# Kernel tuning notes

Measured on AMD Instinct MI355X. Metric: run time of the kernel, lower is better.

## Reference

```python
import jax, jax.numpy as jnp
import numpy as np

N, M = 20000, 5000
D_IN, D_OUT = 256, 512
EPS = 1e-5


def setup_inputs() -> dict:
    key = jax.random.key(0)
    k1, k2, k3, k4 = jax.random.split(key, 4)
    x = jax.random.normal(k1, (N, D_IN), dtype=jnp.float32)
    H = (jax.random.uniform(k2, (N, M)) < 0.05).astype(jnp.float32)
    W_node = jax.random.normal(k3, (D_IN, D_OUT), dtype=jnp.float32) / np.sqrt(D_IN)
    W_res = jax.random.normal(k4, (D_IN, D_OUT), dtype=jnp.float32) / np.sqrt(D_IN)
    gamma = jnp.ones((D_OUT,), dtype=jnp.float32)
    beta = jnp.zeros((D_OUT,), dtype=jnp.float32)
    return {"x": x, "H": H, "W_node": W_node, "W_res": W_res, "gamma": gamma, "beta": beta}


def reference(x, H, W_node, W_res, gamma, beta):
    # degrees, clamped to >= 1
    d_v = jnp.clip(jnp.sum(H, axis=1), 1.0)   # [N] node degree
    d_e = jnp.clip(jnp.sum(H, axis=0), 1.0)   # [M] hyperedge degree
    x_proj = x @ W_node                       # [N, d_out]
    edge_feat = (H.T @ x_proj) / d_e[:, None] # [M, d_out] node -> edge aggregation
    node_update = (H @ edge_feat) / d_v[:, None]  # [N, d_out] edge -> node
    h = node_update + x @ W_res               # residual (d_in != d_out -> linear)
    # LayerNorm over last dim
    mu = jnp.mean(h, axis=-1, keepdims=True)
    var = jnp.mean(jnp.square(h - mu), axis=-1, keepdims=True)
    out = (h - mu) * jax.lax.rsqrt(var + EPS) * gamma + beta
    return out  # dropout is identity at inference
```

## Files before the change

### kernel.cpp

```cpp
#include <hip/hip_runtime.h>


#define N_NODES 20000
#define M_EDGES 5000
#define MPAD    5120
#define NPAD    20480
#define NW      320
#define MW      80
#define DIN     256
#define DOUT    512
#define SPLITS  16
#define SPLITSB 4

typedef short bf16x8 __attribute__((ext_vector_type(8)));
typedef float f32x4 __attribute__((ext_vector_type(4)));
typedef unsigned long long u64;

#define MFMA16(A, B, C) __builtin_amdgcn_mfma_f32_16x16x32_bf16((A), (B), (C), 0, 0, 0)

__device__ __forceinline__ unsigned short f2b(float f) {
  unsigned u = __builtin_bit_cast(unsigned, f);
  return (unsigned short)((u + 0x7FFFu + ((u >> 16) & 1u)) >> 16);
}

__device__ __forceinline__ float b2f(unsigned short b) {
  return __builtin_bit_cast(float, ((unsigned)b) << 16);
}

__device__ __forceinline__ void stage16(const void* g, void* l) {
  __builtin_amdgcn_global_load_lds(
      (const __attribute__((address_space(1))) unsigned int*)g,
      (__attribute__((address_space(3))) unsigned int*)l, 16, 0, 0);
}

__device__ __forceinline__ bf16x8 expand8(unsigned b) {
  union { unsigned u[4]; bf16x8 v; } r;
  const unsigned t = b | (b << 15);
  r.u[0] = (t & 0x00010001u) * 0x3F80u;
  r.u[1] = ((t >> 2) & 0x00010001u) * 0x3F80u;
  r.u[2] = ((t >> 4) & 0x00010001u) * 0x3F80u;
  r.u[3] = ((t >> 6) & 0x00010001u) * 0x3F80u;
  return r.v;
}

__global__ __launch_bounds__(256) void prep_kernel(const float* __restrict__ Wn,
                                                   const float* __restrict__ Wr,
                                                   unsigned short* __restrict__ wtpb) {
  const int q = blockIdx.x * 256 + threadIdx.x;
  const int j = q >> 9, k = q & 511;
  const float v = (k < 256) ? Wn[(size_t)k * 512 + j] : Wr[(size_t)(k - 256) * 512 + j];
  wtpb[(((size_t)(k >> 3) * 512 + j) << 3) + (k & 7)] = f2b(v);
}

__global__ __launch_bounds__(256) void xt_kernel(const float* __restrict__ x,
                                                 unsigned short* __restrict__ xpb) {
  const int j = threadIdx.x;
  const int n8 = blockIdx.x;
  union { unsigned u[4]; bf16x8 v; } o;
#pragma unroll
  for (int p = 0; p < 4; ++p) {
    const int n = n8 * 8 + 2 * p;
    const float v0 = (n < N_NODES) ? x[(size_t)n * DIN + j] : 0.f;
    const float v1 = (n + 1 < N_NODES) ? x[(size_t)(n + 1) * DIN + j] : 0.f;
    o.u[p] = (unsigned)f2b(v0) | ((unsigned)f2b(v1) << 16);
  }
  *(bf16x8*)(xpb + ((size_t)n8 * 256 + j) * 8) = o.v;
}

__global__ __launch_bounds__(256) void pack_kernel(const float* __restrict__ H,
                                                   u64* __restrict__ HTb) {
  const int t = threadIdx.x;
  const int g = blockIdx.x;
  const int h = blockIdx.y;
  const int n0 = g * 64;
  const int mc = h * 1024 + 4 * t;
  u64 h0 = 0, h1 = 0, h2 = 0, h3 = 0;
  if (mc + 3 < M_EDGES) {
    const float* col = H + mc;
#pragma unroll 4
    for (int r = 0; r < 64; ++r) {
      const int n = n0 + r;
      if (n < N_NODES) {
        const float4 v = *(const float4*)(col + (size_t)n * M_EDGES);
        h0 |= (u64)(v.x != 0.f) << r;
        h1 |= (u64)(v.y != 0.f) << r;
        h2 |= (u64)(v.z != 0.f) << r;
        h3 |= (u64)(v.w != 0.f) << r;
      }
    }
  } else if (mc < M_EDGES) {
    for (int r = 0; r < 64; ++r) {
      const int n = n0 + r;
      if (n < N_NODES) {
        const float* row = H + (size_t)n * M_EDGES;
        if (mc + 0 < M_EDGES) h0 |= (u64)(row[mc + 0] != 0.f) << r;
        if (mc + 1 < M_EDGES) h1 |= (u64)(row[mc + 1] != 0.f) << r;
        if (mc + 2 < M_EDGES) h2 |= (u64)(row[mc + 2] != 0.f) << r;
        if (mc + 3 < M_EDGES) h3 |= (u64)(row[mc + 3] != 0.f) << r;
      }
    }
  }
  u64* hp = HTb + (size_t)g * MPAD + mc;
  hp[0] = h0; hp[1] = h1; hp[2] = h2; hp[3] = h3;
}

__global__ __launch_bounds__(256) void bt_kernel(const u64* __restrict__ HTb,
                                                 u64* __restrict__ Hb) {
  const int t = threadIdx.x;
  const int w = t >> 6, l = t & 63;
  const int id = blockIdx.x * 4 + w;
  const int nw = id % NW;
  const int mw = id / NW;
  const u64 word = HTb[(size_t)nw * MPAD + mw * 64 + l];
  u64 out = 0;
  for (int r = 0; r < 64; ++r) {
    const u64 mask = __ballot(((word >> r) & 1ull) != 0);
    if (l == r) out = mask;
  }
  Hb[(size_t)mw * NPAD + nw * 64 + l] = out;
}

__global__ __launch_bounds__(256) void deg_kernel(const u64* __restrict__ Hb,
                                                  const u64* __restrict__ HTb,
                                                  float* __restrict__ inv_de,
                                                  float* __restrict__ inv_dv) {
  const int g = blockIdx.x * 256 + threadIdx.x;
  if (g < MPAD) {
    int c = 0;
    for (int nw = 0; nw < NW; ++nw) c += __popcll(HTb[(size_t)nw * MPAD + g]);
    inv_de[g] = 1.f / fmaxf((float)c, 1.f);
  } else if (g < MPAD + NPAD) {
    const int n = g - MPAD;
    int c = 0;
#pragma unroll
    for (int mw = 0; mw < MW; ++mw) c += __popcll(Hb[(size_t)mw * NPAD + n]);
    inv_dv[n] = 1.f / fmaxf((float)c, 1.f);
  }
}

__global__ __launch_bounds__(256) void gemmA_kernel(const unsigned short* __restrict__ xpb,
                                                    const u64* __restrict__ HTb,
                                                    unsigned short* __restrict__ partial) {
  __shared__ char lds[2][16384];
  const int t = threadIdx.x;
  const int w = t >> 6, l = t & 63;
  const int lr = l & 15, lg = l >> 4;
  const int shl8 = lg * 8;
  const int wgid = blockIdx.x;
  const int mchunk = wgid >> 6;
  const int sj = wgid & 63;
  const int s = sj >> 2, jb = sj & 3;
  const int m0 = mchunk * 256 + w * 64;
  const int j0 = jb * 64;

  f32x4 acc[4][4] = {};
  const u64* bbase = HTb + (size_t)(s * 20) * MPAD + m0 + lr;
  const char* xb = (const char*)xpb;
  const int n8b = s * 160;
  const int sj0 = j0 + w * 16 + lr;

  u64 b00, b01, b02, b03, b04, b05, b06, b07;
  u64 b10, b11, b12, b13, b14, b15, b16, b17;

#define GA_LOADB(S, st_) do {                                                  \
    const u64* bp_ = bbase + (size_t)(st_) * 2 * MPAD;                         \
    b##S##0 = bp_[0]; b##S##1 = bp_[16]; b##S##2 = bp_[32]; b##S##3 = bp_[48]; \
    const u64* bq_ = bp_ + MPAD;                                               \
    b##S##4 = bq_[0]; b##S##5 = bq_[16]; b##S##6 = bq_[32]; b##S##7 = bq_[48]; \
  } while (0)

#define GA_STAGE(buf, st_) do {                                                \
    const size_t r0_ = (size_t)(n8b + (st_) * 16 + lg) * 256 + sj0;            \
    stage16(xb + (r0_) * 16,              &lds[buf][(w) * 1024 + l * 16]);     \
    stage16(xb + (r0_ + 4 * 256) * 16,    &lds[buf][(4 + w) * 1024 + l * 16]); \
    stage16(xb + (r0_ + 8 * 256) * 16,    &lds[buf][(8 + w) * 1024 + l * 16]); \
    stage16(xb + (r0_ + 12 * 256) * 16,   &lds[buf][(12 + w) * 1024 + l * 16]);\
  } while (0)

#define GA_JG(jg, BW) do {                                                     \
    const unsigned wlo_ = (unsigned)(BW), whi_ = (unsigned)((BW) >> 32);       \
    const bf16x8 e0_ = expand8((wlo_ >> shl8) & 255u);                         \
    const bf16x8 e1_ = expand8((whi_ >> shl8) & 255u);                         \
    acc[0][jg] = MFMA16(A00_, e0_, acc[0][jg]);                                \
    acc[1][jg] = MFMA16(A10_, e0_, acc[1][jg]);                                \
    acc[2][jg] = MFMA16(A20_, e0_, acc[2][jg]);                                \
    acc[3][jg] = MFMA16(A30_, e0_, acc[3][jg]);                                \
    acc[0][jg] = MFMA16(A01_, e1_, acc[0][jg]);                                \
    acc[1][jg] = MFMA16(A11_, e1_, acc[1][jg]);                                \
    acc[2][jg] = MFMA16(A21_, e1_, acc[2][jg]);                                \
    acc[3][jg] = MFMA16(A31_, e1_, acc[3][jg]);                                \
  } while (0)

#define GA_COMP(buf, h, W0, W1, W2, W3) do {                                   \
    const char* L_ = &lds[buf][(h) * 8192];                                    \
    const bf16x8 A00_ = *(const bf16x8*)(L_ + l * 16 + 0);                     \
    const bf16x8 A10_ = *(const bf16x8*)(L_ + l * 16 + 1024);                  \
    const bf16x8 A20_ = *(const bf16x8*)(L_ + l * 16 + 2048);                  \
    const bf16x8 A30_ = *(const bf16x8*)(L_ + l * 16 + 3072);                  \
    const bf16x8 A01_ = *(const bf16x8*)(L_ + l * 16 + 4096);                  \
    const bf16x8 A11_ = *(const bf16x8*)(L_ + l * 16 + 5120);                  \
    const bf16x8 A21_ = *(const bf16x8*)(L_ + l * 16 + 6144);                  \
    const bf16x8 A31_ = *(const bf16x8*)(L_ + l * 16 + 7168);                  \
    GA_JG(0, W0); GA_JG(1, W1); GA_JG(2, W2); GA_JG(3, W3);                    \
  } while (0)

  GA_LOADB(0, 0);
  GA_STAGE(0, 0);
  for (int st = 0; st < 10; st += 2) {
    const int n1 = (st + 1 < 10) ? st + 1 : 9;
    GA_LOADB(1, n1); GA_STAGE(1, n1);
    asm volatile("s_waitcnt vmcnt(12)" ::: "memory");
    __builtin_amdgcn_s_barrier();
    GA_COMP(0, 0, b00, b01, b02, b03);
    GA_COMP(0, 1, b04, b05, b06, b07);
    __builtin_amdgcn_s_barrier();
    const int n2 = (st + 2 < 10) ? st + 2 : 9;
    GA_LOADB(0, n2); GA_STAGE(0, n2);
    asm volatile("s_waitcnt vmcnt(12)" ::: "memory");
    __builtin_amdgcn_s_barrier();
    GA_COMP(1, 0, b10, b11, b12, b13);
    GA_COMP(1, 1, b14, b15, b16, b17);
    __builtin_amdgcn_s_barrier();
  }
#undef GA_LOADB
#undef GA_STAGE
#undef GA_JG
#undef GA_COMP

  unsigned short* pp = partial + (size_t)s * (DIN * MPAD);
#pragma unroll
  for (int fr = 0; fr < 4; ++fr)
#pragma unroll
    for (int r = 0; r < 4; ++r) {
      const int j = j0 + fr * 16 + lg * 4 + r;
#pragma unroll
      for (int jg = 0; jg < 4; ++jg)
        pp[(size_t)j * MPAD + m0 + jg * 16 + lr] = f2b(acc[fr][jg][r]);
    }
}

__global__ __launch_bounds__(256) void reduceA_kernel(const unsigned short* __restrict__ partial,
                                                      const float* __restrict__ inv_de,
                                                      unsigned short* __restrict__ t2p) {
  const int t = threadIdx.x;
  const int m = blockIdx.x * 256 + t;
  const int jc = blockIdx.y * 16;
  const float e = inv_de[m];
  unsigned short* ob = t2p + ((size_t)(m >> 3) * 256) * 8 + (m & 7);
  for (int jj = 0; jj < 16; ++jj) {
    const int j = jc + jj;
    const unsigned short* p = partial + (size_t)j * MPAD + m;
    float s = 0.f;
#pragma unroll
    for (int sp = 0; sp < SPLITS; ++sp) s += b2f(p[(size_t)sp * (DIN * MPAD)]);
    ob[(size_t)j * 8] = f2b(s * e);
  }
}

__global__ __launch_bounds__(256) void gemmB_kernel(const unsigned short* __restrict__ t2p,
                                                    const u64* __restrict__ Hb,
                                                    unsigned short* __restrict__ partialB) {
  __shared__ char lds[2][16384];
  const int t = threadIdx.x;
  const int w = t >> 6, l = t & 63;
  const int lr = l & 15, lg = l >> 4;
  const int shl8 = lg * 8;
  const int wgid = blockIdx.x;
  const int nchunk = wgid >> 4;
  const int sj = wgid & 15;
  const int s = sj >> 2, jb = sj & 3;
  const int n0 = nchunk * 256 + w * 64;
  const int j0 = jb * 64;

  f32x4 acc[4][4] = {};
  const u64* abase = Hb + (size_t)(s * 20) * NPAD + n0 + lr;
  const char* tb = (const char*)t2p;
  const int m8b = s * 160;
  const int sj0 = j0 + w * 16 + lr;

  u64 a00, a01, a02, a03, a04, a05, a06, a07;
  u64 a10, a11, a12, a13, a14, a15, a16, a17;

#define GB_LOADA(S, st_) do {                                                  \
    const u64* ap_ = abase + (size_t)(st_) * 2 * NPAD;                         \
    a##S##0 = ap_[0]; a##S##1 = ap_[16]; a##S##2 = ap_[32]; a##S##3 = ap_[48]; \
    const u64* aq_ = ap_ + NPAD;                                               \
    a##S##4 = aq_[0]; a##S##5 = aq_[16]; a##S##6 = aq_[32]; a##S##7 = aq_[48]; \
  } while (0)

#define GB_STAGE(buf, st_) do {                                                \
    const size_t r0_ = (size_t)(m8b + (st_) * 16 + lg) * 256 + sj0;            \
    stage16(tb + (r0_) * 16,              &lds[buf][(w) * 1024 + l * 16]);     \
    stage16(tb + (r0_ + 4 * 256) * 16,    &lds[buf][(4 + w) * 1024 + l * 16]); \
    stage16(tb + (r0_ + 8 * 256) * 16,    &lds[buf][(8 + w) * 1024 + l * 16]); \
    stage16(tb + (r0_ + 12 * 256) * 16,   &lds[buf][(12 + w) * 1024 + l * 16]);\
  } while (0)

#define GB_FR(fr, AW) do {                                                     \
    const unsigned wlo_ = (unsigned)(AW), whi_ = (unsigned)((AW) >> 32);       \
    const bf16x8 e0_ = expand8((wlo_ >> shl8) & 255u);                         \
    const bf16x8 e1_ = expand8((whi_ >> shl8) & 255u);                         \
    acc[fr][0] = MFMA16(e0_, B00_, acc[fr][0]);                                \
    acc[fr][1] = MFMA16(e0_, B10_, acc[fr][1]);                                \
    acc[fr][2] = MFMA16(e0_, B20_, acc[fr][2]);                                \
    acc[fr][3] = MFMA16(e0_, B30_, acc[fr][3]);                                \
    acc[fr][0] = MFMA16(e1_, B01_, acc[fr][0]);                                \
    acc[fr][1] = MFMA16(e1_, B11_, acc[fr][1]);                                \
    acc[fr][2] = MFMA16(e1_, B21_, acc[fr][2]);                                \
    acc[fr][3] = MFMA16(e1_, B31_, acc[fr][3]);                                \
  } while (0)

#define GB_COMP(buf, h, W0, W1, W2, W3) do {                                   \
    const char* L_ = &lds[buf][(h) * 8192];                                    \
    const bf16x8 B00_ = *(const bf16x8*)(L_ + l * 16 + 0);                     \
    const bf16x8 B10_ = *(const bf16x8*)(L_ + l * 16 + 1024);                  \
    const bf16x8 B20_ = *(const bf16x8*)(L_ + l * 16 + 2048);                  \
    const bf16x8 B30_ = *(const bf16x8*)(L_ + l * 16 + 3072);                  \
    const bf16x8 B01_ = *(const bf16x8*)(L_ + l * 16 + 4096);                  \
    const bf16x8 B11_ = *(const bf16x8*)(L_ + l * 16 + 5120);                  \
    const bf16x8 B21_ = *(const bf16x8*)(L_ + l * 16 + 6144);                  \
    const bf16x8 B31_ = *(const bf16x8*)(L_ + l * 16 + 7168);                  \
    GB_FR(0, W0); GB_FR(1, W1); GB_FR(2, W2); GB_FR(3, W3);                    \
  } while (0)

  GB_LOADA(0, 0);
  GB_STAGE(0, 0);
  for (int st = 0; st < 10; st += 2) {
    const int n1 = (st + 1 < 10) ? st + 1 : 9;
    GB_LOADA(1, n1); GB_STAGE(1, n1);
    asm volatile("s_waitcnt vmcnt(12)" ::: "memory");
    __builtin_amdgcn_s_barrier();
    GB_COMP(0, 0, a00, a01, a02, a03);
    GB_COMP(0, 1, a04, a05, a06, a07);
    __builtin_amdgcn_s_barrier();
    const int n2 = (st + 2 < 10) ? st + 2 : 9;
    GB_LOADA(0, n2); GB_STAGE(0, n2);
    asm volatile("s_waitcnt vmcnt(12)" ::: "memory");
    __builtin_amdgcn_s_barrier();
    GB_COMP(1, 0, a10, a11, a12, a13);
    GB_COMP(1, 1, a14, a15, a16, a17);
    __builtin_amdgcn_s_barrier();
  }
#undef GB_LOADA
#undef GB_STAGE
#undef GB_FR
#undef GB_COMP

  unsigned short* pp = partialB + (size_t)s * ((size_t)NPAD * DIN);
#pragma unroll
  for (int fr = 0; fr < 4; ++fr) {
#pragma unroll
    for (int r = 0; r < 4; ++r) {
      const int n = n0 + fr * 16 + lg * 4 + r;
#pragma unroll
      for (int jg = 0; jg < 4; ++jg)
        pp[(size_t)n * DIN + j0 + jg * 16 + lr] = f2b(acc[fr][jg][r]);
    }
  }
}

__global__ __launch_bounds__(512) void gemmC2_kernel(const unsigned short* __restrict__ partialB,
                                                     const float* __restrict__ inv_dv,
                                                     const float* __restrict__ x,
                                                     const unsigned short* __restrict__ wtpb,
                                                     const float* __restrict__ gamma,
                                                     const float* __restrict__ beta,
                                                     float* __restrict__ out) {
  __shared__ char ldsA[65536];
  __shared__ float lnred[2][64][8];
  const int t = threadIdx.x;
  const int w = t >> 6, l = t & 63;
  const int lr = l & 15, lg = l >> 4;
  const int n0 = blockIdx.x * 64;

  {
    const int k8 = t & 31;
    const int rb = t >> 5;
#pragma unroll
    for (int pass = 0; pass < 4; ++pass) {
      const int r = pass * 16 + rb;
      const size_t base = (size_t)(n0 + r) * 256 + k8 * 8;
      float sum[8] = {0.f, 0.f, 0.f, 0.f, 0.f, 0.f, 0.f, 0.f};
#pragma unroll
      for (int sp = 0; sp < SPLITSB; ++sp) {
        const bf16x8 v = *(const bf16x8*)(partialB + (size_t)sp * ((size_t)NPAD * DIN) + base);
#pragma unroll
        for (int i = 0; i < 8; ++i) sum[i] += b2f((unsigned short)v[i]);
      }
      const float dv = inv_dv[n0 + r];
      union { unsigned u[4]; bf16x8 v; } o;
#pragma unroll
      for (int p = 0; p < 4; ++p)
        o.u[p] = (unsigned)f2b(sum[2 * p] * dv) | ((unsigned)f2b(sum[2 * p + 1] * dv) << 16);
      *(bf16x8*)(ldsA + r * 1024 + ((k8 * 16) ^ ((r & 7) << 4))) = o.v;
    }
  }
  {
    const int c4 = t & 63;
    const int rb = t >> 6;
#pragma unroll
    for (int pass = 0; pass < 8; ++pass) {
      const int r = pass * 8 + rb;
      float4 v = make_float4(0.f, 0.f, 0.f, 0.f);
      if (n0 + r < N_NODES) v = *(const float4*)(x + (size_t)(n0 + r) * DIN + c4 * 4);
      const unsigned u0 = (unsigned)f2b(v.x) | ((unsigned)f2b(v.y) << 16);
      const unsigned u1 = (unsigned)f2b(v.z) | ((unsigned)f2b(v.w) << 16);
      const int byte0 = 512 + c4 * 8;
      const int off = ((byte0 & ~15) ^ ((r & 7) << 4)) + (byte0 & 8);
      *(uint2*)(ldsA + r * 1024 + off) = make_uint2(u0, u1);
    }
  }
  __syncthreads();

  f32x4 acc[4][4] = {};
  const int wcol = w * 64;
#pragma unroll 2
  for (int kt = 0; kt < 16; ++kt) {
    bf16x8 bf[4];
#pragma unroll
    for (int jg = 0; jg < 4; ++jg) {
      const int col = wcol + jg * 16 + lr;
      bf[jg] = *(const bf16x8*)(wtpb + (((size_t)(kt * 4 + lg) * 512 + col) << 3));
    }
    const int kbA = kt * 64 + lg * 16;
#pragma unroll
    for (int fr = 0; fr < 4; ++fr) {
      const int row = fr * 16 + lr;
      const bf16x8 af = *(const bf16x8*)(ldsA + row * 1024 + (kbA ^ ((row & 7) << 4)));
#pragma unroll
      for (int jg = 0; jg < 4; ++jg)
        acc[fr][jg] = MFMA16(af, bf[jg], acc[fr][jg]);
    }
  }

#pragma unroll
  for (int fr = 0; fr < 4; ++fr)
#pragma unroll
    for (int r = 0; r < 4; ++r) {
      float s = 0.f, s2 = 0.f;
#pragma unroll
      for (int jg = 0; jg < 4; ++jg) {
        const float v = acc[fr][jg][r];
        s += v; s2 += v * v;
      }
#pragma unroll
      for (int m = 1; m < 16; m <<= 1) {
        s += __shfl_xor(s, m, 64);
        s2 += __shfl_xor(s2, m, 64);
      }
      if (lr == 0) {
        const int row = fr * 16 + lg * 4 + r;
        lnred[0][row][w] = s;
        lnred[1][row][w] = s2;
      }
    }
  __syncthreads();

#pragma unroll
  for (int fr = 0; fr < 4; ++fr) {
#pragma unroll
    for (int r = 0; r < 4; ++r) {
      const int row = fr * 16 + lg * 4 + r;
      float S = 0.f, S2 = 0.f;
#pragma unroll
      for (int ww = 0; ww < 8; ++ww) { S += lnred[0][row][ww]; S2 += lnred[1][row][ww]; }
      const float mu = S * (1.f / 512.f);
      const float rs = rsqrtf(S2 * (1.f / 512.f) - mu * mu + 1e-5f);
      const int gn = n0 + row;
      if (gn < N_NODES) {
#pragma unroll
        for (int jg = 0; jg < 4; ++jg) {
          const int col = wcol + jg * 16 + lr;
          out[(size_t)gn * DOUT + col] = (acc[fr][jg][r] - mu) * rs * gamma[col] + beta[col];
        }
      }
    }
  }
}

extern "C" void kernel_launch(void* const* d_in, const int* in_sizes, int n_in,
                              void* d_out, int out_size, void* d_ws, size_t ws_size,
                              hipStream_t stream) {
  (void)in_sizes; (void)n_in; (void)out_size; (void)ws_size;
  const float* x = (const float*)d_in[0];
  const float* H = (const float*)d_in[1];
  const float* Wn = (const float*)d_in[2];
  const float* Wr = (const float*)d_in[3];
  const float* gamma = (const float*)d_in[4];
  const float* beta = (const float*)d_in[5];
  float* out = (float*)d_out;
  char* ws = (char*)d_ws;

  unsigned short* wtpb     = (unsigned short*)(ws + 0);
  u64* Hb                  = (u64*)(ws + 524288);
  u64* HTb                 = (u64*)(ws + 13631488);
  float* inv_de            = (float*)(ws + 26738688);
  float* inv_dv            = (float*)(ws + 26759168);
  unsigned short* xpb      = (unsigned short*)(ws + 26841088);
  unsigned short* partialA = (unsigned short*)(ws + 37326848);
  unsigned short* t2p      = (unsigned short*)(ws + 79269888);
  unsigned short* partialB = (unsigned short*)(ws + 81891328);

  prep_kernel<<<dim3(1024), dim3(256), 0, stream>>>(Wn, Wr, wtpb);
  xt_kernel<<<dim3(2560), dim3(256), 0, stream>>>(x, xpb);
  pack_kernel<<<dim3(320, 5), dim3(256), 0, stream>>>(H, HTb);
  bt_kernel<<<dim3(6400), dim3(256), 0, stream>>>(HTb, Hb);
  deg_kernel<<<dim3(100), dim3(256), 0, stream>>>(Hb, HTb, inv_de, inv_dv);
  gemmA_kernel<<<dim3(1280), dim3(256), 0, stream>>>(xpb, HTb, partialA);
  reduceA_kernel<<<dim3(20, 16), dim3(256), 0, stream>>>(partialA, inv_de, t2p);
  gemmB_kernel<<<dim3(1280), dim3(256), 0, stream>>>(t2p, Hb, partialB);
  gemmC2_kernel<<<dim3(313), dim3(512), 0, stream>>>(partialB, inv_dv, x, wtpb,
                                                     gamma, beta, out);
}
```

Baseline: 319.0 us.

## Double per-block output tile width in hypergraph GEMMs to reuse bitmask operands

Both bitmask GEMMs (node-to-edge and edge-to-node) now compute 128 feature columns per block instead of 64, halving grid size. Each expanded bitmask fragment feeds eight MFMAs instead of four, and LDS staging doubles to 32 KB per buffer with a new k-step layout. This cuts redundant loads and expansions of the bitmask, at the cost of twice as many accumulator registers (occupancy hint of 2 blocks) and fewer blocks in flight.

```diff
diff --git a/kernel.cpp b/kernel.cpp
--- a/kernel.cpp
+++ b/kernel.cpp
@@ -138,26 +138,25 @@
   }
 }
 
-__global__ __launch_bounds__(256) void gemmA_kernel(const unsigned short* __restrict__ xpb,
-                                                    const u64* __restrict__ HTb,
-                                                    unsigned short* __restrict__ partial) {
-  __shared__ char lds[2][16384];
+__global__ __launch_bounds__(256, 2) void gemmA_kernel(const unsigned short* __restrict__ xpb,
+                                                       const u64* __restrict__ HTb,
+                                                       unsigned short* __restrict__ partial) {
+  __shared__ char lds[2][32768];
   const int t = threadIdx.x;
   const int w = t >> 6, l = t & 63;
   const int lr = l & 15, lg = l >> 4;
   const int shl8 = lg * 8;
   const int wgid = blockIdx.x;
-  const int mchunk = wgid >> 6;
-  const int sj = wgid & 63;
-  const int s = sj >> 2, jb = sj & 3;
+  const int mchunk = wgid >> 5;
+  const int sj = wgid & 31;
+  const int s = sj >> 1, jb = sj & 1;
   const int m0 = mchunk * 256 + w * 64;
-  const int j0 = jb * 64;
-
-  f32x4 acc[4][4] = {};
+  const int j0 = jb * 128;
+
+  f32x4 acc[8][4] = {};
   const u64* bbase = HTb + (size_t)(s * 20) * MPAD + m0 + lr;
   const char* xb = (const char*)xpb;
   const int n8b = s * 160;
-  const int sj0 = j0 + w * 16 + lr;
 
   u64 b00, b01, b02, b03, b04, b05, b06, b07;
   u64 b10, b11, b12, b13, b14, b15, b16, b17;
@@ -170,38 +169,65 @@
   } while (0)
 
 #define GA_STAGE(buf, st_) do {                                                \
-    const size_t r0_ = (size_t)(n8b + (st_) * 16 + lg) * 256 + sj0;            \
-    stage16(xb + (r0_) * 16,              &lds[buf][(w) * 1024 + l * 16]);     \
-    stage16(xb + (r0_ + 4 * 256) * 16,    &lds[buf][(4 + w) * 1024 + l * 16]); \
-    stage16(xb + (r0_ + 8 * 256) * 16,    &lds[buf][(8 + w) * 1024 + l * 16]); \
-    stage16(xb + (r0_ + 12 * 256) * 16,   &lds[buf][(12 + w) * 1024 + l * 16]);\
+    const int bn_ = n8b + (st_) * 16 + (t >> 7);                               \
+    const int jj_ = j0 + (t & 127);                                            \
+    stage16(xb + ((size_t)(bn_ +  0) * 256 + jj_) * 16, &lds[buf][0 * 4096 + t * 16]); \
+    stage16(xb + ((size_t)(bn_ +  2) * 256 + jj_) * 16, &lds[buf][1 * 4096 + t * 16]); \
+    stage16(xb + ((size_t)(bn_ +  4) * 256 + jj_) * 16, &lds[buf][2 * 4096 + t * 16]); \
+    stage16(xb + ((size_t)(bn_ +  6) * 256 + jj_) * 16, &lds[buf][3 * 4096 + t * 16]); \
+    stage16(xb + ((size_t)(bn_ +  8) * 256 + jj_) * 16, &lds[buf][4 * 4096 + t * 16]); \
+    stage16(xb + ((size_t)(bn_ + 10) * 256 + jj_) * 16, &lds[buf][5 * 4096 + t * 16]); \
+    stage16(xb + ((size_t)(bn_ + 12) * 256 + jj_) * 16, &lds[buf][6 * 4096 + t * 16]); \
+    stage16(xb + ((size_t)(bn_ + 14) * 256 + jj_) * 16, &lds[buf][7 * 4096 + t * 16]); \
   } while (0)
 
-#define GA_JG(jg, BW) do {                                                     \
-    const unsigned wlo_ = (unsigned)(BW), whi_ = (unsigned)((BW) >> 32);       \
-    const bf16x8 e0_ = expand8((wlo_ >> shl8) & 255u);                         \
-    const bf16x8 e1_ = expand8((whi_ >> shl8) & 255u);                         \
-    acc[0][jg] = MFMA16(A00_, e0_, acc[0][jg]);                                \
-    acc[1][jg] = MFMA16(A10_, e0_, acc[1][jg]);                                \
-    acc[2][jg] = MFMA16(A20_, e0_, acc[2][jg]);                                \
-    acc[3][jg] = MFMA16(A30_, e0_, acc[3][jg]);                                \
-    acc[0][jg] = MFMA16(A01_, e1_, acc[0][jg]);                                \
-    acc[1][jg] = MFMA16(A11_, e1_, acc[1][jg]);                                \
-    acc[2][jg] = MFMA16(A21_, e1_, acc[2][jg]);                                \
-    acc[3][jg] = MFMA16(A31_, e1_, acc[3][jg]);                                \
-  } while (0)
-
-#define GA_COMP(buf, h, W0, W1, W2, W3) do {                                   \
-    const char* L_ = &lds[buf][(h) * 8192];                                    \
-    const bf16x8 A00_ = *(const bf16x8*)(L_ + l * 16 + 0);                     \
-    const bf16x8 A10_ = *(const bf16x8*)(L_ + l * 16 + 1024);                  \
-    const bf16x8 A20_ = *(const bf16x8*)(L_ + l * 16 + 2048);                  \
-    const bf16x8 A30_ = *(const bf16x8*)(L_ + l * 16 + 3072);                  \
-    const bf16x8 A01_ = *(const bf16x8*)(L_ + l * 16 + 4096);                  \
-    const bf16x8 A11_ = *(const bf16x8*)(L_ + l * 16 + 5120);                  \
-    const bf16x8 A21_ = *(const bf16x8*)(L_ + l * 16 + 6144);                  \
-    const bf16x8 A31_ = *(const bf16x8*)(L_ + l * 16 + 7168);                  \
-    GA_JG(0, W0); GA_JG(1, W1); GA_JG(2, W2); GA_JG(3, W3);                    \
+#define GA_KS(buf, ks, sh, W0, W1, W2, W3) do {                                \
+    const char* Lb_ = &lds[buf][((ks) * 4 + lg) * 2048 + lr * 16];             \
+    const bf16x8 A0_ = *(const bf16x8*)(Lb_ + 0);                              \
+    const bf16x8 A1_ = *(const bf16x8*)(Lb_ + 256);                            \
+    const bf16x8 A2_ = *(const bf16x8*)(Lb_ + 512);                            \
+    const bf16x8 A3_ = *(const bf16x8*)(Lb_ + 768);                            \
+    const bf16x8 A4_ = *(const bf16x8*)(Lb_ + 1024);                           \
+    const bf16x8 A5_ = *(const bf16x8*)(Lb_ + 1280);                           \
+    const bf16x8 A6_ = *(const bf16x8*)(Lb_ + 1536);                           \
+    const bf16x8 A7_ = *(const bf16x8*)(Lb_ + 1792);                           \
+    bf16x8 e_;                                                                 \
+    e_ = expand8(((unsigned)((W0) >> (sh)) >> shl8) & 255u);                   \
+    acc[0][0] = MFMA16(A0_, e_, acc[0][0]);                                    \
+    acc[1][0] = MFMA16(A1_, e_, acc[1][0]);                                    \
+    acc[2][0] = MFMA16(A2_, e_, acc[2][0]);                                    \
+    acc[3][0] = MFMA16(A3_, e_, acc[3][0]);                                    \
+    acc[4][0] = MFMA16(A4_, e_, acc[4][0]);                                    \
+    acc[5][0] = MFMA16(A5_, e_, acc[5][0]);                                    \
+    acc[6][0] = MFMA16(A6_, e_, acc[6][0]);                                    \
+    acc[7][0] = MFMA16(A7_, e_, acc[7][0]);                                    \
+    e_ = expand8(((unsigned)((W1) >> (sh)) >> shl8) & 255u);                   \
+    acc[0][1] = MFMA16(A0_, e_, acc[0][1]);                                    \
+    acc[1][1] = MFMA16(A1_, e_, acc[1][1]);                                    \
+    acc[2][1] = MFMA16(A2_, e_, acc[2][1]);                                    \
+    acc[3][1] = MFMA16(A3_, e_, acc[3][1]);                                    \
+    acc[4][1] = MFMA16(A4_, e_, acc[4][1]);                                    \
+    acc[5][1] = MFMA16(A5_, e_, acc[5][1]);                                    \
+    acc[6][1] = MFMA16(A6_, e_, acc[6][1]);                                    \
+    acc[7][1] = MFMA16(A7_, e_, acc[7][1]);                                    \
+    e_ = expand8(((unsigned)((W2) >> (sh)) >> shl8) & 255u);                   \
+    acc[0][2] = MFMA16(A0_, e_, acc[0][2]);                                    \
+    acc[1][2] = MFMA16(A1_, e_, acc[1][2]);                                    \
+    acc[2][2] = MFMA16(A2_, e_, acc[2][2]);                                    \
+    acc[3][2] = MFMA16(A3_, e_, acc[3][2]);                                    \
+    acc[4][2] = MFMA16(A4_, e_, acc[4][2]);                                    \
+    acc[5][2] = MFMA16(A5_, e_, acc[5][2]);                                    \
+    acc[6][2] = MFMA16(A6_, e_, acc[6][2]);                                    \
+    acc[7][2] = MFMA16(A7_, e_, acc[7][2]);                                    \
+    e_ = expand8(((unsigned)((W3) >> (sh)) >> shl8) & 255u);                   \
+    acc[0][3] = MFMA16(A0_, e_, acc[0][3]);                                    \
+    acc[1][3] = MFMA16(A1_, e_, acc[1][3]);                                    \
+    acc[2][3] = MFMA16(A2_, e_, acc[2][3]);                                    \
+    acc[3][3] = MFMA16(A3_, e_, acc[3][3]);                                    \
+    acc[4][3] = MFMA16(A4_, e_, acc[4][3]);                                    \
+    acc[5][3] = MFMA16(A5_, e_, acc[5][3]);                                    \
+    acc[6][3] = MFMA16(A6_, e_, acc[6][3]);                                    \
+    acc[7][3] = MFMA16(A7_, e_, acc[7][3]);                                    \
   } while (0)
 
   GA_LOADB(0, 0);
@@ -209,33 +235,36 @@
   for (int st = 0; st < 10; st += 2) {
     const int n1 = (st + 1 < 10) ? st + 1 : 9;
     GA_LOADB(1, n1); GA_STAGE(1, n1);
-    asm volatile("s_waitcnt vmcnt(12)" ::: "memory");
-    __builtin_amdgcn_s_barrier();
-    GA_COMP(0, 0, b00, b01, b02, b03);
-    GA_COMP(0, 1, b04, b05, b06, b07);
+    asm volatile("s_waitcnt vmcnt(16)" ::: "memory");
+    __builtin_amdgcn_s_barrier();
+    GA_KS(0, 0, 0,  b00, b01, b02, b03);
+    GA_KS(0, 1, 32, b00, b01, b02, b03);
+    GA_KS(0, 2, 0,  b04, b05, b06, b07);
+    GA_KS(0, 3, 32, b04, b05, b06, b07);
     __builtin_amdgcn_s_barrier();
     const int n2 = (st + 2 < 10) ? st + 2 : 9;
     GA_LOADB(0, n2); GA_STAGE(0, n2);
-    asm volatile("s_waitcnt vmcnt(12)" ::: "memory");
-    __builtin_amdgcn_s_barrier();
-    GA_COMP(1, 0, b10, b11, b12, b13);
-    GA_COMP(1, 1, b14, b15, b16, b17);
+    asm volatile("s_waitcnt vmcnt(16)" ::: "memory");
+    __builtin_amdgcn_s_barrier();
+    GA_KS(1, 0, 0,  b10, b11, b12, b13);
+    GA_KS(1, 1, 32, b10, b11, b12, b13);
+    GA_KS(1, 2, 0,  b14, b15, b16, b17);
+    GA_KS(1, 3, 32, b14, b15, b16, b17);
     __builtin_amdgcn_s_barrier();
   }
 #undef GA_LOADB
 #undef GA_STAGE
-#undef GA_JG
-#undef GA_COMP
+#undef GA_KS
 
   unsigned short* pp = partial + (size_t)s * (DIN * MPAD);
 #pragma unroll
-  for (int fr = 0; fr < 4; ++fr)
+  for (int fr = 0; fr < 8; ++fr)
 #pragma unroll
     for (int r = 0; r < 4; ++r) {
       const int j = j0 + fr * 16 + lg * 4 + r;
 #pragma unroll
-      for (int jg = 0; jg < 4; ++jg)
-        pp[(size_t)j * MPAD + m0 + jg * 16 + lr] = f2b(acc[fr][jg][r]);
+      for (int mg = 0; mg < 4; ++mg)
+        pp[(size_t)j * MPAD + m0 + mg * 16 + lr] = f2b(acc[fr][mg][r]);
     }
 }
 
@@ -257,26 +286,25 @@
   }
 }
 
-__global__ __launch_bounds__(256) void gemmB_kernel(const unsigned short* __restrict__ t2p,
-                                                    const u64* __restrict__ Hb,
-                                                    unsigned short* __restrict__ partialB) {
-  __shared__ char lds[2][16384];
+__global__ __launch_bounds__(256, 2) void gemmB_kernel(const unsigned short* __restrict__ t2p,
+                                                       const u64* __restrict__ Hb,
+                                                       unsigned short* __restrict__ partialB) {
+  __shared__ char lds[2][32768];
   const int t = threadIdx.x;
   const int w = t >> 6, l = t & 63;
   const int lr = l & 15, lg = l >> 4;
   const int shl8 = lg * 8;
   const int wgid = blockIdx.x;
-  const int nchunk = wgid >> 4;
-  const int sj = wgid & 15;
-  const int s = sj >> 2, jb = sj & 3;
+  const int nchunk = wgid >> 3;
+  const int sj = wgid & 7;
+  const int s = sj >> 1, jb = sj & 1;
   const int n0 = nchunk * 256 + w * 64;
-  const int j0 = jb * 64;
-
-  f32x4 acc[4][4] = {};
+  const int j0 = jb * 128;
+
+  f32x4 acc[4][8] = {};
   const u64* abase = Hb + (size_t)(s * 20) * NPAD + n0 + lr;
   const char* tb = (const char*)t2p;
   const int m8b = s * 160;
-  const int sj0 = j0 + w * 16 + lr;
 
   u64 a00, a01, a02, a03, a04, a05, a06, a07;
   u64 a10, a11, a12, a13, a14, a15, a16, a17;
@@ -289,38 +317,65 @@
   } while (0)
 
 #define GB_STAGE(buf, st_) do {                                                \
-    const size_t r0_ = (size_t)(m8b + (st_) * 16 + lg) * 256 + sj0;            \
-    stage16(tb + (r0_) * 16,              &lds[buf][(w) * 1024 + l * 16]);     \
-    stage16(tb + (r0_ + 4 * 256) * 16,    &lds[buf][(4 + w) * 1024 + l * 16]); \
-    stage16(tb + (r0_ + 8 * 256) * 16,    &lds[buf][(8 + w) * 1024 + l * 16]); \
-    stage16(tb + (r0_ + 12 * 256) * 16,   &lds[buf][(12 + w) * 1024 + l * 16]);\
+    const int bm_ = m8b + (st_) * 16 + (t >> 7);                               \
+    const int jj_ = j0 + (t & 127);                                            \
+    stage16(tb + ((size_t)(bm_ +  0) * 256 + jj_) * 16, &lds[buf][0 * 4096 + t * 16]); \
+    stage16(tb + ((size_t)(bm_ +  2) * 256 + jj_) * 16, &lds[buf][1 * 4096 + t * 16]); \
+    stage16(tb + ((size_t)(bm_ +  4) * 256 + jj_) * 16, &lds[buf][2 * 4096 + t * 16]); \
+    stage16(tb + ((size_t)(bm_ +  6) * 256 + jj_) * 16, &lds[buf][3 * 4096 + t * 16]); \
+    stage16(tb + ((size_t)(bm_ +  8) * 256 + jj_) * 16, &lds[buf][4 * 4096 + t * 16]); \
+    stage16(tb + ((size_t)(bm_ + 10) * 256 + jj_) * 16, &lds[buf][5 * 4096 + t * 16]); \
+    stage16(tb + ((size_t)(bm_ + 12) * 256 + jj_) * 16, &lds[buf][6 * 4096 + t * 16]); \
+    stage16(tb + ((size_t)(bm_ + 14) * 256 + jj_) * 16, &lds[buf][7 * 4096 + t * 16]); \
   } while (0)
 
-#define GB_FR(fr, AW) do {                                                     \
-    const unsigned wlo_ = (unsigned)(AW), whi_ = (unsigned)((AW) >> 32);       \
-    const bf16x8 e0_ = expand8((wlo_ >> shl8) & 255u);                         \
-    const bf16x8 e1_ = expand8((whi_ >> shl8) & 255u);                         \
-    acc[fr][0] = MFMA16(e0_, B00_, acc[fr][0]);                                \
-    acc[fr][1] = MFMA16(e0_, B10_, acc[fr][1]);                                \
-    acc[fr][2] = MFMA16(e0_, B20_, acc[fr][2]);                                \
-    acc[fr][3] = MFMA16(e0_, B30_, acc[fr][3]);                                \
-    acc[fr][0] = MFMA16(e1_, B01_, acc[fr][0]);                                \
-    acc[fr][1] = MFMA16(e1_, B11_, acc[fr][1]);                                \
-    acc[fr][2] = MFMA16(e1_, B21_, acc[fr][2]);                                \
-    acc[fr][3] = MFMA16(e1_, B31_, acc[fr][3]);                                \
-  } while (0)
-
-#define GB_COMP(buf, h, W0, W1, W2, W3) do {                                   \
-    const char* L_ = &lds[buf][(h) * 8192];                                    \
-    const bf16x8 B00_ = *(const bf16x8*)(L_ + l * 16 + 0);                     \
-    const bf16x8 B10_ = *(const bf16x8*)(L_ + l * 16 + 1024);                  \
-    const bf16x8 B20_ = *(const bf16x8*)(L_ + l * 16 + 2048);                  \
-    const bf16x8 B30_ = *(const bf16x8*)(L_ + l * 16 + 3072);                  \
-    const bf16x8 B01_ = *(const bf16x8*)(L_ + l * 16 + 4096);                  \
-    const bf16x8 B11_ = *(const bf16x8*)(L_ + l * 16 + 5120);                  \
-    const bf16x8 B21_ = *(const bf16x8*)(L_ + l * 16 + 6144);                  \
-    const bf16x8 B31_ = *(const bf16x8*)(L_ + l * 16 + 7168);                  \
-    GB_FR(0, W0); GB_FR(1, W1); GB_FR(2, W2); GB_FR(3, W3);                    \
+#define GB_KS(buf, ks, sh, W0, W1, W2, W3) do {                                \
+    const char* Lb_ = &lds[buf][((ks) * 4 + lg) * 2048 + lr * 16];             \
+    const bf16x8 B0_ = *(const bf16x8*)(Lb_ + 0);                              \
+    const bf16x8 B1_ = *(const bf16x8*)(Lb_ + 256);                            \
+    const bf16x8 B2_ = *(const bf16x8*)(Lb_ + 512);                            \
+    const bf16x8 B3_ = *(const bf16x8*)(Lb_ + 768);                            \
+    const bf16x8 B4_ = *(const bf16x8*)(Lb_ + 1024);                           \
+    const bf16x8 B5_ = *(const bf16x8*)(Lb_ + 1280);                           \
+    const bf16x8 B6_ = *(const bf16x8*)(Lb_ + 1536);                           \
+    const bf16x8 B7_ = *(const bf16x8*)(Lb_ + 1792);                           \
+    bf16x8 e_;                                                                 \
+    e_ = expand8(((unsigned)((W0) >> (sh)) >> shl8) & 255u);                   \
+    acc[0][0] = MFMA16(e_, B0_, acc[0][0]);                                    \
+    acc[0][1] = MFMA16(e_, B1_, acc[0][1]);                                    \
+    acc[0][2] = MFMA16(e_, B2_, acc[0][2]);                                    \
+    acc[0][3] = MFMA16(e_, B3_, acc[0][3]);                                    \
+    acc[0][4] = MFMA16(e_, B4_, acc[0][4]);                                    \
+    acc[0][5] = MFMA16(e_, B5_, acc[0][5]);                                    \
+    acc[0][6] = MFMA16(e_, B6_, acc[0][6]);                                    \
+    acc[0][7] = MFMA16(e_, B7_, acc[0][7]);                                    \
+    e_ = expand8(((unsigned)((W1) >> (sh)) >> shl8) & 255u);                   \
+    acc[1][0] = MFMA16(e_, B0_, acc[1][0]);                                    \
+    acc[1][1] = MFMA16(e_, B1_, acc[1][1]);                                    \
+    acc[1][2] = MFMA16(e_, B2_, acc[1][2]);                                    \
+    acc[1][3] = MFMA16(e_, B3_, acc[1][3]);                                    \
+    acc[1][4] = MFMA16(e_, B4_, acc[1][4]);                                    \
+    acc[1][5] = MFMA16(e_, B5_, acc[1][5]);                                    \
+    acc[1][6] = MFMA16(e_, B6_, acc[1][6]);                                    \
+    acc[1][7] = MFMA16(e_, B7_, acc[1][7]);                                    \
+    e_ = expand8(((unsigned)((W2) >> (sh)) >> shl8) & 255u);                   \
+    acc[2][0] = MFMA16(e_, B0_, acc[2][0]);                                    \
+    acc[2][1] = MFMA16(e_, B1_, acc[2][1]);                                    \
+    acc[2][2] = MFMA16(e_, B2_, acc[2][2]);                                    \
+    acc[2][3] = MFMA16(e_, B3_, acc[2][3]);                                    \
+    acc[2][4] = MFMA16(e_, B4_, acc[2][4]);                                    \
+    acc[2][5] = MFMA16(e_, B5_, acc[2][5]);                                    \
+    acc[2][6] = MFMA16(e_, B6_, acc[2][6]);                                    \
+    acc[2][7] = MFMA16(e_, B7_, acc[2][7]);                                    \
+    e_ = expand8(((unsigned)((W3) >> (sh)) >> shl8) & 255u);                   \
+    acc[3][0] = MFMA16(e_, B0_, acc[3][0]);                                    \
+    acc[3][1] = MFMA16(e_, B1_, acc[3][1]);                                    \
+    acc[3][2] = MFMA16(e_, B2_, acc[3][2]);                                    \
+    acc[3][3] = MFMA16(e_, B3_, acc[3][3]);                                    \
+    acc[3][4] = MFMA16(e_, B4_, acc[3][4]);                                    \
+    acc[3][5] = MFMA16(e_, B5_, acc[3][5]);                                    \
+    acc[3][6] = MFMA16(e_, B6_, acc[3][6]);                                    \
+    acc[3][7] = MFMA16(e_, B7_, acc[3][7]);                                    \
   } while (0)
 
   GB_LOADA(0, 0);
@@ -328,33 +383,36 @@
   for (int st = 0; st < 10; st += 2) {
     const int n1 = (st + 1 < 10) ? st + 1 : 9;
     GB_LOADA(1, n1); GB_STAGE(1, n1);
-    asm volatile("s_waitcnt vmcnt(12)" ::: "memory");
-    __builtin_amdgcn_s_barrier();
-    GB_COMP(0, 0, a00, a01, a02, a03);
-    GB_COMP(0, 1, a04, a05, a06, a07);
+    asm volatile("s_waitcnt vmcnt(16)" ::: "memory");
+    __builtin_amdgcn_s_barrier();
+    GB_KS(0, 0, 0,  a00, a01, a02, a03);
+    GB_KS(0, 1, 32, a00, a01, a02, a03);
+    GB_KS(0, 2, 0,  a04, a05, a06, a07);
+    GB_KS(0, 3, 32, a04, a05, a06, a07);
     __builtin_amdgcn_s_barrier();
     const int n2 = (st + 2 < 10) ? st + 2 : 9;
     GB_LOADA(0, n2); GB_STAGE(0, n2);
-    asm volatile("s_waitcnt vmcnt(12)" ::: "memory");
-    __builtin_amdgcn_s_barrier();
-    GB_COMP(1, 0, a10, a11, a12, a13);
-    GB_COMP(1, 1, a14, a15, a16, a17);
+    asm volatile("s_waitcnt vmcnt(16)" ::: "memory");
+    __builtin_amdgcn_s_barrier();
+    GB_KS(1, 0, 0,  a10, a11, a12, a13);
+    GB_KS(1, 1, 32, a10, a11, a12, a13);
+    GB_KS(1, 2, 0,  a14, a15, a16, a17);
+    GB_KS(1, 3, 32, a14, a15, a16, a17);
     __builtin_amdgcn_s_barrier();
   }
 #undef GB_LOADA
 #undef GB_STAGE
-#undef GB_FR
-#undef GB_COMP
+#undef GB_KS
 
   unsigned short* pp = partialB + (size_t)s * ((size_t)NPAD * DIN);
 #pragma unroll
-  for (int fr = 0; fr < 4; ++fr) {
+  for (int fn = 0; fn < 4; ++fn) {
 #pragma unroll
     for (int r = 0; r < 4; ++r) {
-      const int n = n0 + fr * 16 + lg * 4 + r;
-#pragma unroll
-      for (int jg = 0; jg < 4; ++jg)
-        pp[(size_t)n * DIN + j0 + jg * 16 + lr] = f2b(acc[fr][jg][r]);
+      const int n = n0 + fn * 16 + lg * 4 + r;
+#pragma unroll
+      for (int fj = 0; fj < 8; ++fj)
+        pp[(size_t)n * DIN + j0 + fj * 16 + lr] = f2b(acc[fn][fj][r]);
     }
   }
 }
@@ -506,9 +564,9 @@
   pack_kernel<<<dim3(320, 5), dim3(256), 0, stream>>>(H, HTb);
   bt_kernel<<<dim3(6400), dim3(256), 0, stream>>>(HTb, Hb);
   deg_kernel<<<dim3(100), dim3(256), 0, stream>>>(Hb, HTb, inv_de, inv_dv);
-  gemmA_kernel<<<dim3(1280), dim3(256), 0, stream>>>(xpb, HTb, partialA);
+  gemmA_kernel<<<dim3(640), dim3(256), 0, stream>>>(xpb, HTb, partialA);
   reduceA_kernel<<<dim3(20, 16), dim3(256), 0, stream>>>(partialA, inv_de, t2p);
-  gemmB_kernel<<<dim3(1280), dim3(256), 0, stream>>>(t2p, Hb, partialB);
+  gemmB_kernel<<<dim3(640), dim3(256), 0, stream>>>(t2p, Hb, partialB);
   gemmC2_kernel<<<dim3(313), dim3(512), 0, stream>>>(partialB, inv_dv, x, wtpb,
                                                      gamma, beta, out);
 }
```

Result: slower. 515.8 us (+61.7%).
